# Kernel tuning notes

Hardware: AMD Instinct MI355X
Metric: run time of the kernel (lower is better)

Reference implementation:

```python
import jax, jax.numpy as jnp
import numpy as np

T, H = 8192, 2048


def setup_inputs() -> dict:
    key = jax.random.key(0)
    k1, k2, k3 = jax.random.split(key, 3)
    x_sequence = jax.random.normal(k1, (T, H), dtype=jnp.float32)
    lamda = jax.random.normal(k2, (H,), dtype=jnp.float32) * 0.2
    B = jax.random.normal(k3, (H, H), dtype=jnp.float32) / np.sqrt(H).astype(np.float32)
    return {"x_sequence": x_sequence, "lamda": lamda, "B": B}


def reference(x_sequence, lamda, B):
    # Batched input projection: u_t = B @ x_t for all t -> one GEMM. [T, H]
    u = x_sequence @ B.T
    # Linear diagonal recurrence h_t = lamda * h_{t-1} + u_t with h_0 = 0,
    # solved with a log-depth associative scan over (a, b) pairs where
    # combine((a1,b1),(a2,b2)) = (a2*a1, a2*b1 + b2).
    a = jnp.broadcast_to(lamda, u.shape)  # [T, H]

    def combine(c1, c2):
        a1, b1 = c1
        a2, b2 = c2
        return (a2 * a1, a2 * b1 + b2)

    _, h = jax.lax.associative_scan(combine, (a, u))
    return h  # [T, H] stacked hidden states
```

## Files before the change

kernel.cpp:

```cpp
#include <hip/hip_runtime.h>
#include <hip/hip_bf16.h>


#define TDIM 8192
#define HDIM 2048
#define BM 256
#define BN 256
#define BK 32
#define NT (HDIM / BK)
#define ASLOT 8192
#define BSLOT 8192
#define LCH 64
#define GCH (TDIM / LCH)

#define XBF_BYTES (TDIM * HDIM * 2)
#define BBF_BYTES (HDIM * HDIM * 2)
#define E_BYTES   (GCH * HDIM * 4)
#define WS_NEED   ((size_t)XBF_BYTES + BBF_BYTES + E_BYTES)

typedef float f32x4 __attribute__((ext_vector_type(4)));
typedef short s16x4 __attribute__((ext_vector_type(4)));
typedef short s16x8 __attribute__((ext_vector_type(8)));

static __device__ __forceinline__ short f2bf(float f) {
  __bf16 b = (__bf16)f;
  return __builtin_bit_cast(short, b);
}

#define SB()   asm volatile("s_barrier" ::: "memory")
#define VMW(n) asm volatile("s_waitcnt vmcnt(" #n ")" ::: "memory")
#define GL(gp, lp)                                                            \
  __builtin_amdgcn_global_load_lds(                                           \
      (const __attribute__((address_space(1))) void*)(gp),                    \
      (__attribute__((address_space(3))) void*)(lp), 16, 0, 0)

__global__ void cvt_fast(const float* __restrict__ X, const float* __restrict__ Bm,
                         short* __restrict__ Xb, short* __restrict__ Bb) {
  const int XN4 = TDIM * HDIM / 4;
  const int BN4 = HDIM * HDIM / 4;
  const int stride = gridDim.x * blockDim.x;
  for (int i = blockIdx.x * blockDim.x + threadIdx.x; i < XN4 + BN4; i += stride) {
    const float* s;
    short* d;
    int k;
    if (i < XN4) { s = X;  d = Xb; k = i; }
    else         { s = Bm; d = Bb; k = i - XN4; }
    f32x4 v = *(const f32x4*)(s + (size_t)k * 4);
    s16x4 o;
    o[0] = f2bf(v[0]); o[1] = f2bf(v[1]); o[2] = f2bf(v[2]); o[3] = f2bf(v[3]);
    *(s16x4*)(d + (size_t)k * 4) = o;
  }
}

__global__ __launch_bounds__(512, 2) void gemm8p2(
    const short* __restrict__ Xb, const short* __restrict__ Bb,
    float* __restrict__ U) {
  extern __shared__ __align__(16) short smem[];
  short* As = smem;
  short* Bs = smem + 4 * ASLOT;

  const int wg  = blockIdx.x;
  const int swz = (wg & 7) * 32 + (wg >> 3);
  const int tm = swz >> 3;
  const int tn = swz & 7;
  const int row0 = tm * BM, col0 = tn * BN;

  const int tid  = threadIdx.x;
  const int lane = tid & 63;
  const int wid  = tid >> 6;
  const int wr = (wid >> 2) * 128;
  const int wc = (wid & 3) * 64;
  const int r16 = lane & 15;
  const int ks8 = (lane >> 4) * 8;

  int offA[8], offB[4];
#pragma unroll
  for (int m = 0; m < 8; ++m) {
    const int r = wr + m * 16 + r16;
    offA[m] = r * BK + (ks8 ^ (((r >> 1) & 3) * 8));
  }
#pragma unroll
  for (int n = 0; n < 4; ++n) {
    const int r = wc + n * 16 + r16;
    offB[n] = r * BK + (ks8 ^ (((r >> 1) & 3) * 8));
  }

  const int srow = tid >> 2;
  const int sg   = (tid & 3) ^ ((tid >> 3) & 3);
  const short* gA0 = Xb + (size_t)(row0 + srow) * HDIM + sg * 8;
  const short* gA1 = gA0 + (size_t)128 * HDIM;
  const short* gB0 = Bb + (size_t)(col0 + srow) * HDIM + sg * 8;
  const short* gB1 = gB0 + (size_t)128 * HDIM;

  f32x4 acc[8][4] = {};

#pragma unroll
  for (int k = 0; k < 3; ++k) {
    GL(gA0 + k * BK, &As[k * ASLOT + tid * 8]);
    GL(gA1 + k * BK, &As[k * ASLOT + 4096 + tid * 8]);
    GL(gB0 + k * BK, &Bs[k * BSLOT + tid * 8]);
    GL(gB1 + k * BK, &Bs[k * BSLOT + 4096 + tid * 8]);
  }
  VMW(8);
  SB();

#define ITER(J_, ST_, VMA_, SBF_) do {                                        \
    const int sc_ = (J_) & 3;                                                 \
    const int si_ = ((J_) + 3) & 3;                                           \
    const int ko_ = ((J_) + 3) * BK;                                          \
    s16x8 af[4], bfv[4];                                                      \
    _Pragma("unroll") for (int m = 0; m < 4; ++m)                             \
      af[m] = *(const s16x8*)&As[sc_ * ASLOT + offA[m]];                      \
    _Pragma("unroll") for (int n = 0; n < 4; ++n)                             \
      bfv[n] = *(const s16x8*)&Bs[sc_ * BSLOT + offB[n]];                     \
    if (ST_) {                                                                \
      GL(gA0 + ko_, &As[si_ * ASLOT + tid * 8]);                              \
      GL(gA1 + ko_, &As[si_ * ASLOT + 4096 + tid * 8]);                       \
    }                                                                         \
    SB();                                                                     \
    __builtin_amdgcn_s_setprio(1);                                            \
    _Pragma("unroll") for (int m = 0; m < 4; ++m)                             \
      _Pragma("unroll") for (int n = 0; n < 4; ++n)                           \
        acc[m][n] = __builtin_amdgcn_mfma_f32_16x16x32_bf16(                  \
            af[m], bfv[n], acc[m][n], 0, 0, 0);                               \
    __builtin_amdgcn_s_setprio(0);                                            \
    SB();                                                                     \
    _Pragma("unroll") for (int m = 0; m < 4; ++m)                             \
      af[m] = *(const s16x8*)&As[sc_ * ASLOT + offA[4 + m]];                  \
    if (ST_) {                                                                \
      GL(gB0 + ko_, &Bs[si_ * BSLOT + tid * 8]);                              \
      GL(gB1 + ko_, &Bs[si_ * BSLOT + 4096 + tid * 8]);                       \
    }                                                                         \
    SB();                                                                     \
    __builtin_amdgcn_s_setprio(1);                                            \
    _Pragma("unroll") for (int m = 0; m < 4; ++m)                             \
      _Pragma("unroll") for (int n = 0; n < 4; ++n)                           \
        acc[4 + m][n] = __builtin_amdgcn_mfma_f32_16x16x32_bf16(              \
            af[m], bfv[n], acc[4 + m][n], 0, 0, 0);                           \
    __builtin_amdgcn_s_setprio(0);                                            \
    VMA_;                                                                     \
    SBF_;                                                                     \
  } while (0)

#pragma unroll 4
  for (int j = 0; j < NT - 4; ++j) ITER(j, true, VMW(8), SB());
  ITER(NT - 4, true,  VMW(8), SB());
  ITER(NT - 3, false, VMW(4), SB());
  ITER(NT - 2, false, VMW(0), SB());
  ITER(NT - 1, false, (void)0, (void)0);
#undef ITER

  const int crow = row0 + wr + ((lane >> 4) << 2);
  const int ccol = col0 + wc + r16;
#pragma unroll
  for (int m = 0; m < 8; ++m)
#pragma unroll
    for (int n = 0; n < 4; ++n)
#pragma unroll
      for (int j = 0; j < 4; ++j)
        U[(size_t)(crow + m * 16 + j) * HDIM + ccol + n * 16] = acc[m][n][j];
}

__global__ __launch_bounds__(256, 2) void gemm_f32_fb(
    const float* __restrict__ X, const float* __restrict__ Bm,
    float* __restrict__ U) {
#define LDK 40
#define FBM 128
#define FBK 32
#define FNT (HDIM / FBK)
  __shared__ __align__(16) short As[2][FBM * LDK];
  __shared__ __align__(16) short Bs[2][FBM * LDK];
  const int wg  = blockIdx.x;
  const int cpx = (TDIM / FBM) * (HDIM / FBM) / 8;
  const int swz = (wg & 7) * cpx + (wg >> 3);
  const int tm = swz >> 4;
  const int tn = swz & 15;
  const int row0 = tm * FBM, col0 = tn * FBM;
  const int tid  = threadIdx.x;
  const int lane = tid & 63;
  const int wid  = tid >> 6;
  const int wr = (wid >> 1) * 64;
  const int wc = (wid & 1) * 64;
  const int srow = tid >> 2;
  const int sk   = (tid & 3) << 3;
  const float* gA  = X  + (size_t)(row0 + srow) * HDIM + sk;
  const float* gA2 = gA + 64 * HDIM;
  const float* gB  = Bm + (size_t)(col0 + srow) * HDIM + sk;
  const float* gB2 = gB + 64 * HDIM;
  f32x4 a00, a01, a10, a11, b00, b01, b10, b11;
#define LOADREG(kt) do {                                                      \
    const float* p;                                                           \
    p = gA  + (kt) * FBK; a00 = *(const f32x4*)p; a01 = *(const f32x4*)(p+4); \
    p = gA2 + (kt) * FBK; a10 = *(const f32x4*)p; a11 = *(const f32x4*)(p+4); \
    p = gB  + (kt) * FBK; b00 = *(const f32x4*)p; b01 = *(const f32x4*)(p+4); \
    p = gB2 + (kt) * FBK; b10 = *(const f32x4*)p; b11 = *(const f32x4*)(p+4); \
  } while (0)
#define CVT8(v, lo, hi) do {                                                  \
    v[0] = f2bf(lo[0]); v[1] = f2bf(lo[1]); v[2] = f2bf(lo[2]);               \
    v[3] = f2bf(lo[3]); v[4] = f2bf(hi[0]); v[5] = f2bf(hi[1]);               \
    v[6] = f2bf(hi[2]); v[7] = f2bf(hi[3]);                                   \
  } while (0)
#define DSWRITE(buf) do {                                                     \
    s16x8 v;                                                                  \
    CVT8(v, a00, a01); *(s16x8*)&As[buf][srow * LDK + sk] = v;                \
    CVT8(v, a10, a11); *(s16x8*)&As[buf][(srow + 64) * LDK + sk] = v;         \
    CVT8(v, b00, b01); *(s16x8*)&Bs[buf][srow * LDK + sk] = v;                \
    CVT8(v, b10, b11); *(s16x8*)&Bs[buf][(srow + 64) * LDK + sk] = v;         \
  } while (0)
  f32x4 acc[4][4] = {};
#define COMPUTE(buf) do {                                                     \
    const int r16_ = lane & 15;                                               \
    const int ks_  = (lane >> 4) * 8;                                         \
    s16x8 af[4], bfr[4];                                                      \
    _Pragma("unroll") for (int m = 0; m < 4; ++m)                             \
      af[m] = *(const s16x8*)&As[buf][(wr + m * 16 + r16_) * LDK + ks_];      \
    _Pragma("unroll") for (int n = 0; n < 4; ++n)                             \
      bfr[n] = *(const s16x8*)&Bs[buf][(wc + n * 16 + r16_) * LDK + ks_];     \
    _Pragma("unroll") for (int m = 0; m < 4; ++m)                             \
      _Pragma("unroll") for (int n = 0; n < 4; ++n)                           \
        acc[m][n] = __builtin_amdgcn_mfma_f32_16x16x32_bf16(                  \
            af[m], bfr[n], acc[m][n], 0, 0, 0);                               \
  } while (0)
  LOADREG(0);
  DSWRITE(0);
  __syncthreads();
#pragma unroll 2
  for (int kt = 0; kt < FNT; ++kt) {
    const int cur = kt & 1;
    if (kt + 1 < FNT) LOADREG(kt + 1);
    COMPUTE(cur);
    if (kt + 1 < FNT) DSWRITE(cur ^ 1);
    __syncthreads();
  }
  const int crow = wr + ((lane >> 4) << 2);
  const int ccol = wc + (lane & 15);
#pragma unroll
  for (int m = 0; m < 4; ++m)
#pragma unroll
    for (int n = 0; n < 4; ++n)
#pragma unroll
      for (int j = 0; j < 4; ++j)
        U[(size_t)(row0 + crow + m * 16 + j) * HDIM + (col0 + ccol + n * 16)] =
            acc[m][n][j];
#undef LOADREG
#undef CVT8
#undef DSWRITE
#undef COMPUTE
#undef LDK
#undef FBM
#undef FBK
#undef FNT
}

__global__ void scan_pass1(const float* __restrict__ U,
                           const float* __restrict__ lam,
                           float* __restrict__ e) {
  const int c = (blockIdx.y * 256 + threadIdx.x) * 4;
  const int j = blockIdx.x;
  const f32x4 l4 = *(const f32x4*)&lam[c];
  f32x4 h = {0.f, 0.f, 0.f, 0.f};
  const float* up = U + (size_t)j * LCH * HDIM + c;
#pragma unroll 4
  for (int t = 0; t < LCH; ++t) {
    f32x4 u4 = *(const f32x4*)up;
    h = l4 * h + u4;
    up += HDIM;
  }
  *(f32x4*)&e[(size_t)j * HDIM + c] = h;
}

__global__ void scan_carry(float* __restrict__ e, const float* __restrict__ lam) {
  const int c = (blockIdx.x * 256 + threadIdx.x) * 4;
  const f32x4 l4 = *(const f32x4*)&lam[c];
  f32x4 p = l4;
#pragma unroll
  for (int i = 0; i < 6; ++i) p = p * p;
  f32x4 E = {0.f, 0.f, 0.f, 0.f};
  for (int j = 0; j < GCH; ++j) {
    f32x4 ej = *(const f32x4*)&e[(size_t)j * HDIM + c];
    *(f32x4*)&e[(size_t)j * HDIM + c] = E;
    E = p * E + ej;
  }
}

__global__ void scan_pass3(float* __restrict__ U, const float* __restrict__ lam,
                           const float* __restrict__ carry) {
  const int c = (blockIdx.y * 256 + threadIdx.x) * 4;
  const int j = blockIdx.x;
  const f32x4 l4 = *(const f32x4*)&lam[c];
  f32x4 h = *(const f32x4*)&carry[(size_t)j * HDIM + c];
  float* up = U + (size_t)j * LCH * HDIM + c;
#pragma unroll 4
  for (int t = 0; t < LCH; ++t) {
    f32x4 u4 = *(const f32x4*)up;
    h = l4 * h + u4;
    *(f32x4*)up = h;
    up += HDIM;
  }
}

extern "C" void kernel_launch(void* const* d_in, const int* in_sizes, int n_in,
                              void* d_out, int out_size, void* d_ws, size_t ws_size,
                              hipStream_t stream) {
  const float* X   = (const float*)d_in[0];
  const float* lam = (const float*)d_in[1];
  const float* Bm  = (const float*)d_in[2];
  float* U = (float*)d_out;

  if (ws_size >= WS_NEED) {
    short* Xb = (short*)d_ws;
    short* Bb = (short*)((char*)d_ws + XBF_BYTES);
    float* e  = (float*)((char*)d_ws + XBF_BYTES + BBF_BYTES);

    hipFuncSetAttribute((const void*)gemm8p2,
                        hipFuncAttributeMaxDynamicSharedMemorySize, 131072);

    cvt_fast<<<dim3(2048), dim3(256), 0, stream>>>(X, Bm, Xb, Bb);
    gemm8p2<<<dim3((TDIM / BM) * (HDIM / BN)), dim3(512), 131072, stream>>>(
        Xb, Bb, U);
    scan_pass1<<<dim3(GCH, HDIM / 1024), dim3(256), 0, stream>>>(U, lam, e);
    scan_carry<<<dim3(HDIM / 1024), dim3(256), 0, stream>>>(e, lam);
    scan_pass3<<<dim3(GCH, HDIM / 1024), dim3(256), 0, stream>>>(U, lam, e);
  } else {
    float* e = (float*)d_ws;
    gemm_f32_fb<<<dim3((TDIM / 128) * (HDIM / 128)), dim3(256), 0, stream>>>(
        X, Bm, U);
    scan_pass1<<<dim3(GCH, HDIM / 1024), dim3(256), 0, stream>>>(U, lam, e);
    scan_carry<<<dim3(HDIM / 1024), dim3(256), 0, stream>>>(e, lam);
    scan_pass3<<<dim3(GCH, HDIM / 1024), dim3(256), 0, stream>>>(U, lam, e);
  }
}
```

Before: 128.8 us.

## Fuse bf16 conversion into GEMM kernel with grid-wide atomic barrier

Removes the separate fp32-to-bf16 conversion kernel and performs the conversion at the start of the GEMM kernel, with each of the 256 workgroups converting a slice of X and B. A global atomic counter then acts as a grid barrier before the GEMM main loop, and a memset resets the flag each call. This saves one kernel launch and its tail, but it relies on all 256 workgroups being co-resident (2 per CU) and adds a spin-wait plus a memset.

```diff
diff --git a/kernel.cpp b/kernel.cpp
--- a/kernel.cpp
+++ b/kernel.cpp
@@ -10,13 +10,15 @@
 #define NT (HDIM / BK)
 #define ASLOT 8192
 #define BSLOT 8192
+#define NBLK 256
 #define LCH 64
 #define GCH (TDIM / LCH)
 
 #define XBF_BYTES (TDIM * HDIM * 2)
 #define BBF_BYTES (HDIM * HDIM * 2)
 #define E_BYTES   (GCH * HDIM * 4)
-#define WS_NEED   ((size_t)XBF_BYTES + BBF_BYTES + E_BYTES)
+#define FLAG_OFF  ((size_t)XBF_BYTES + BBF_BYTES + E_BYTES)
+#define WS_NEED   (FLAG_OFF + 64)
 
 typedef float f32x4 __attribute__((ext_vector_type(4)));
 typedef short s16x4 __attribute__((ext_vector_type(4)));
@@ -34,38 +36,59 @@
       (const __attribute__((address_space(1))) void*)(gp),                    \
       (__attribute__((address_space(3))) void*)(lp), 16, 0, 0)
 
-__global__ void cvt_fast(const float* __restrict__ X, const float* __restrict__ Bm,
-                         short* __restrict__ Xb, short* __restrict__ Bb) {
-  const int XN4 = TDIM * HDIM / 4;
-  const int BN4 = HDIM * HDIM / 4;
-  const int stride = gridDim.x * blockDim.x;
-  for (int i = blockIdx.x * blockDim.x + threadIdx.x; i < XN4 + BN4; i += stride) {
-    const float* s;
-    short* d;
-    int k;
-    if (i < XN4) { s = X;  d = Xb; k = i; }
-    else         { s = Bm; d = Bb; k = i - XN4; }
-    f32x4 v = *(const f32x4*)(s + (size_t)k * 4);
-    s16x4 o;
-    o[0] = f2bf(v[0]); o[1] = f2bf(v[1]); o[2] = f2bf(v[2]); o[3] = f2bf(v[3]);
-    *(s16x4*)(d + (size_t)k * 4) = o;
-  }
-}
-
-__global__ __launch_bounds__(512, 2) void gemm8p2(
-    const short* __restrict__ Xb, const short* __restrict__ Bb,
-    float* __restrict__ U) {
+__global__ __launch_bounds__(512, 2) void gemm_one(
+    const float* __restrict__ X, const float* __restrict__ Bm,
+    short* __restrict__ Xb, short* __restrict__ Bb,
+    float* __restrict__ U, int* __restrict__ flag) {
   extern __shared__ __align__(16) short smem[];
   short* As = smem;
   short* Bs = smem + 4 * ASLOT;
 
   const int wg  = blockIdx.x;
+  const int tid = threadIdx.x;
+
+  {
+    const int xcd = wg & 7;
+    const int l   = wg >> 3;
+    const float* xs = X  + (size_t)(xcd * 1024 + l * 32) * HDIM;
+    short*       xd = Xb + (size_t)(xcd * 1024 + l * 32) * HDIM;
+#pragma unroll 4
+    for (int i = 0; i < 32; ++i) {
+      const int idx = i * 512 + tid;
+      f32x4 v = *(const f32x4*)(xs + (size_t)idx * 4);
+      s16x4 o;
+      o[0] = f2bf(v[0]); o[1] = f2bf(v[1]); o[2] = f2bf(v[2]); o[3] = f2bf(v[3]);
+      *(s16x4*)(xd + (size_t)idx * 4) = o;
+    }
+    const float* bs = Bm + (size_t)wg * 16384;
+    short*       bd = Bb + (size_t)wg * 16384;
+#pragma unroll 4
+    for (int i = 0; i < 8; ++i) {
+      const int idx = i * 512 + tid;
+      f32x4 v = *(const f32x4*)(bs + (size_t)idx * 4);
+      s16x4 o;
+      o[0] = f2bf(v[0]); o[1] = f2bf(v[1]); o[2] = f2bf(v[2]); o[3] = f2bf(v[3]);
+      *(s16x4*)(bd + (size_t)idx * 4) = o;
+    }
+  }
+
+  __threadfence();
+  __syncthreads();
+  if (tid == 0) {
+    __hip_atomic_fetch_add(flag, 1, __ATOMIC_ACQ_REL, __HIP_MEMORY_SCOPE_AGENT);
+    while (__hip_atomic_load(flag, __ATOMIC_ACQUIRE, __HIP_MEMORY_SCOPE_AGENT)
+           < NBLK) {
+      __builtin_amdgcn_s_sleep(8);
+    }
+  }
+  __syncthreads();
+  __threadfence();
+
   const int swz = (wg & 7) * 32 + (wg >> 3);
   const int tm = swz >> 3;
   const int tn = swz & 7;
   const int row0 = tm * BM, col0 = tn * BN;
 
-  const int tid  = threadIdx.x;
   const int lane = tid & 63;
   const int wid  = tid >> 6;
   const int wr = (wid >> 2) * 128;
@@ -308,16 +331,16 @@
   float* U = (float*)d_out;
 
   if (ws_size >= WS_NEED) {
-    short* Xb = (short*)d_ws;
-    short* Bb = (short*)((char*)d_ws + XBF_BYTES);
-    float* e  = (float*)((char*)d_ws + XBF_BYTES + BBF_BYTES);
-
-    hipFuncSetAttribute((const void*)gemm8p2,
+    short* Xb  = (short*)d_ws;
+    short* Bb  = (short*)((char*)d_ws + XBF_BYTES);
+    float* e   = (float*)((char*)d_ws + XBF_BYTES + BBF_BYTES);
+    int*   flg = (int*)((char*)d_ws + FLAG_OFF);
+
+    hipFuncSetAttribute((const void*)gemm_one,
                         hipFuncAttributeMaxDynamicSharedMemorySize, 131072);
 
-    cvt_fast<<<dim3(2048), dim3(256), 0, stream>>>(X, Bm, Xb, Bb);
-    gemm8p2<<<dim3((TDIM / BM) * (HDIM / BN)), dim3(512), 131072, stream>>>(
-        Xb, Bb, U);
+    hipMemsetAsync(flg, 0, 64, stream);
+    gemm_one<<<dim3(NBLK), dim3(512), 131072, stream>>>(X, Bm, Xb, Bb, U, flg);
     scan_pass1<<<dim3(GCH, HDIM / 1024), dim3(256), 0, stream>>>(U, lam, e);
     scan_carry<<<dim3(HDIM / 1024), dim3(256), 0, stream>>>(e, lam);
     scan_pass3<<<dim3(GCH, HDIM / 1024), dim3(256), 0, stream>>>(U, lam, e);
```

Result: slower. 238.3 us (+85.1%).
